# Performance work log

Hardware: AMD Instinct MI355X
Metric: run time of the kernel (lower is better)

Reference implementation:

```python
import jax, jax.numpy as jnp
import numpy as np

N_RBF = 20
CUTOFF = 5.0
LN_EPS = 1e-5


def setup_inputs() -> dict:
    key = jax.random.key(0)
    ks = jax.random.split(key, 16)
    N, E, F, H = 20000, 160000, 128, 4
    HF = H * F

    def lin_w(k, fin, fout):
        return (jax.random.normal(k, (fin, fout), jnp.float32) / np.sqrt(fin)).astype(jnp.float32)

    inp = {
        "s_j": jax.random.normal(ks[0], (N, F), jnp.float32),
        "dist": jax.random.uniform(ks[1], (E,), jnp.float32, 0.5, CUTOFF),
        "nbrs": jax.random.randint(ks[2], (E, 2), 0, N),
        # LayerNorm params
        "ln_g": jnp.ones((F,), jnp.float32),
        "ln_b": jnp.zeros((F,), jnp.float32),
        # q/k/v projections: feat_dim -> num_heads*feat_dim
        "Wq": lin_w(ks[3], F, HF), "bq": 0.01 * jax.random.normal(ks[4], (HF,), jnp.float32),
        "Wk": lin_w(ks[5], F, HF), "bk": 0.01 * jax.random.normal(ks[6], (HF,), jnp.float32),
        "Wv": lin_w(ks[7], F, HF), "bv": 0.01 * jax.random.normal(ks[8], (HF,), jnp.float32),
        # RBF -> distance filters dk/dv (Dense with swish activation)
        "dkW": lin_w(ks[9], N_RBF, HF), "dkb": 0.01 * jax.random.normal(ks[10], (HF,), jnp.float32),
        "dvW": lin_w(ks[11], N_RBF, HF), "dvb": 0.01 * jax.random.normal(ks[12], (HF,), jnp.float32),
        # final dense: num_heads*feat_dim -> 3*feat_dim
        "denseW": lin_w(ks[13], HF, 3 * F), "denseb": 0.01 * jax.random.normal(ks[14], (3 * F,), jnp.float32),
    }
    return inp


def reference(s_j, dist, nbrs, ln_g, ln_b, Wq, bq, Wk, bk, Wv, bv, dkW, dkb, dvW, dvb, denseW, denseb):
    F = s_j.shape[-1]
    HF = Wq.shape[-1]
    H = HF // F
    E = dist.shape[0]

    # LayerNorm over feature dim
    mu = s_j.mean(-1, keepdims=True)
    var = ((s_j - mu) ** 2).mean(-1, keepdims=True)
    inp = (s_j - mu) * jax.lax.rsqrt(var + LN_EPS) * ln_g + ln_b  # [N, F]

    # multi-head q/k/v: [N, H, F]
    q = (inp @ Wq + bq).reshape(-1, H, F)
    k = (inp @ Wk + bk).reshape(-1, H, F)
    v = (inp @ Wv + bv).reshape(-1, H, F)

    # Gaussian RBF expansion of distances: [E, n_rbf]
    centers = jnp.linspace(0.0, CUTOFF, N_RBF, dtype=jnp.float32)
    delta = CUTOFF / (N_RBF - 1)
    e_rbf = jnp.exp(-0.5 * ((dist[:, None] - centers) / delta) ** 2)

    # distance filters (Dense + swish): [E, H, F]
    dk = jax.nn.silu(e_rbf @ dkW + dkb).reshape(E, H, F)
    dv = jax.nn.silu(e_rbf @ dvW + dvb).reshape(E, H, F)

    i_idx, j_idx = nbrs[:, 0], nbrs[:, 1]

    # per-edge multi-head attention weight: silu(sum_f q_i * k_j * dk)
    attn = jax.nn.silu(jnp.einsum('ehf,ehf->eh', q[i_idx] * dk, k[j_idx]))  # [E, H]
    env = 0.5 * (jnp.cos(jnp.pi * dist / CUTOFF) + 1.0)  # cosine cutoff envelope [E]

    msg = (attn * env[:, None])[..., None] * v[j_idx] * dv  # [E, H, F]
    out = msg.reshape(E, HF) @ denseW + denseb  # [E, 3F]
    return out.reshape(E, 3, -1)
```

## Files before the change

### kernel.cpp

```cpp
#include <hip/hip_runtime.h>
#include <cstdint>
#include <cstddef>

typedef unsigned short u16;

#define F_DIM   128
#define HF_DIM  512
#define NRBF    20
#define NOUT    384

using bf16x8 = __attribute__((ext_vector_type(8))) __bf16;
using f32x4  = __attribute__((ext_vector_type(4))) float;

__device__ __forceinline__ float bf2f(u16 u){
    union { unsigned int i; float f; } v; v.i = ((unsigned int)u) << 16; return v.f;
}
__device__ __forceinline__ u16 f2bf(float f){
    union { float f; unsigned int i; } v; v.f = f;
    unsigned int x = v.i;
    unsigned int r = x + 0x7fffu + ((x >> 16) & 1u);
    return (u16)(r >> 16);
}
__device__ __forceinline__ float silu(float x){
    return x * __fdividef(1.0f, 1.0f + __expf(-x));
}

__global__ __launch_bounds__(256) void s0_packW(
    const float* __restrict__ dW, u16* __restrict__ Bp)
{
    const int t = blockIdx.x * 256 + threadIdx.x;
    if (t >= 24 * 16 * 64 * 8) return;
    const int j    = t & 7;
    const int lane = (t >> 3) & 63;
    const int ks   = (t >> 9) & 15;
    const int nt   = t >> 13;
    const int k = ks * 32 + ((lane >> 4) << 3) + j;
    const int n = nt * 16 + (lane & 15);
    Bp[t] = f2bf(dW[(size_t)k * NOUT + n]);
}

__global__ __launch_bounds__(128) void s1_ln(
    const float* __restrict__ s_j, const float* __restrict__ ln_g,
    const float* __restrict__ ln_b, float* __restrict__ inp, int N)
{
    __shared__ float ps[2], pss[2];
    const int n = blockIdx.x;
    const int f = threadIdx.x;
    float x = s_j[(size_t)n * F_DIM + f];
    float s = x, ss = x * x;
    #pragma unroll
    for (int o = 1; o < 64; o <<= 1){
        s  += __shfl_xor(s,  o);
        ss += __shfl_xor(ss, o);
    }
    const int wid = f >> 6;
    if ((f & 63) == 0){ ps[wid] = s; pss[wid] = ss; }
    __syncthreads();
    const float S  = ps[0] + ps[1];
    const float SS = pss[0] + pss[1];
    const float mu  = S * (1.f / 128.f);
    const float var = SS * (1.f / 128.f) - mu * mu;
    const float r   = rsqrtf(var + 1e-5f);
    inp[(size_t)n * F_DIM + f] = (x - mu) * r * ln_g[f] + ln_b[f];
}

__global__ __launch_bounds__(512) void s2_qkv(
    const float* __restrict__ inp,
    const float* __restrict__ Wq, const float* __restrict__ bq,
    const float* __restrict__ Wk, const float* __restrict__ bk,
    const float* __restrict__ Wv, const float* __restrict__ bv,
    u16* __restrict__ qo, u16* __restrict__ ko, u16* __restrict__ vo, int N)
{
    __shared__ float a[F_DIM];
    const int n = blockIdx.x;
    const int col = threadIdx.x;
    if (col < F_DIM) a[col] = inp[(size_t)n * F_DIM + col];
    __syncthreads();
    float aq = bq[col], ak = bk[col], av = bv[col];
    for (int k = 0; k < F_DIM; k++){
        const float x = a[k];
        aq += x * Wq[k * HF_DIM + col];
        ak += x * Wk[k * HF_DIM + col];
        av += x * Wv[k * HF_DIM + col];
    }
    qo[(size_t)n * HF_DIM + col] = f2bf(aq);
    ko[(size_t)n * HF_DIM + col] = f2bf(ak);
    vo[(size_t)n * HF_DIM + col] = f2bf(av);
}

__global__ __launch_bounds__(256) void s3_edge_dense(
    const float* __restrict__ dist, const int* __restrict__ nbrs,
    const u16* __restrict__ q_ws, const u16* __restrict__ k_ws, const u16* __restrict__ v_ws,
    const float* __restrict__ dkW, const float* __restrict__ dkb,
    const float* __restrict__ dvW, const float* __restrict__ dvb,
    const u16* __restrict__ Bp, const float* __restrict__ db,
    float* __restrict__ out, int E, int N)
{
    __shared__ __align__(16) u16 msg_s[32][520];
    __shared__ float rbf_sh[32][21];
    __shared__ float env_sh[32];
    const int tid = threadIdx.x;
    const int e0 = blockIdx.x * 32;

    if (tid < 32){
        int de = e0 + tid; if (de >= E) de = E - 1;
        float d = dist[de];
        env_sh[tid] = 0.5f * (__cosf(0.62831853071f * d) + 1.0f);
        const float delta = 5.0f / 19.0f;
        const float invd  = 19.0f / 5.0f;
        #pragma unroll
        for (int r = 0; r < NRBF; r++){
            float t = (d - delta * (float)r) * invd;
            rbf_sh[tid][r] = __expf(-0.5f * t * t);
        }
    }
    __syncthreads();

    {
        const int e_l = tid >> 3, sub = tid & 7;
        const int h = sub >> 1, half = sub & 1;
        const int fb = h * F_DIM + half * 64;
        int e = e0 + e_l; if (e >= E) e = E - 1;
        int i_idx = nbrs[2*e + 0];
        int j_idx = nbrs[2*e + 1];
        i_idx = (i_idx < 0) ? 0 : (i_idx >= N ? N-1 : i_idx);
        j_idx = (j_idx < 0) ? 0 : (j_idx >= N ? N-1 : j_idx);
        float rbf[NRBF];
        #pragma unroll
        for (int r = 0; r < NRBF; r++) rbf[r] = rbf_sh[e_l][r];
        const float env = env_sh[e_l];
        const u16* qrow = q_ws + (size_t)i_idx * HF_DIM + fb;
        const u16* krow = k_ws + (size_t)j_idx * HF_DIM + fb;
        const u16* vrow = v_ws + (size_t)j_idx * HF_DIM + fb;

        float attn = 0.f;
        for (int c = 0; c < 8; c++){
            const int f0 = c * 8;
            float a8[8];
            #pragma unroll
            for (int j = 0; j < 8; j++) a8[j] = dkb[fb + f0 + j];
            #pragma unroll
            for (int r = 0; r < NRBF; r++){
                const float rv = rbf[r];
                const float* wp = dkW + (size_t)r * HF_DIM + fb + f0;
                #pragma unroll
                for (int j = 0; j < 8; j++) a8[j] += rv * wp[j];
            }
            uint4 qu = *(const uint4*)(qrow + f0);
            uint4 ku = *(const uint4*)(krow + f0);
            const u16* qp = (const u16*)&qu;
            const u16* kp = (const u16*)&ku;
            #pragma unroll
            for (int j = 0; j < 8; j++)
                attn += bf2f(qp[j]) * silu(a8[j]) * bf2f(kp[j]);
        }
        attn += __shfl_xor(attn, 1);
        const float scale = silu(attn) * env;

        for (int c = 0; c < 8; c++){
            const int f0 = c * 8;
            float a8[8];
            #pragma unroll
            for (int j = 0; j < 8; j++) a8[j] = dvb[fb + f0 + j];
            #pragma unroll
            for (int r = 0; r < NRBF; r++){
                const float rv = rbf[r];
                const float* wp = dvW + (size_t)r * HF_DIM + fb + f0;
                #pragma unroll
                for (int j = 0; j < 8; j++) a8[j] += rv * wp[j];
            }
            uint4 vu = *(const uint4*)(vrow + f0);
            const u16* vp = (const u16*)&vu;
            u16 ov[8];
            #pragma unroll
            for (int j = 0; j < 8; j++)
                ov[j] = f2bf(scale * bf2f(vp[j]) * silu(a8[j]));
            *(uint4*)&msg_s[e_l][fb + f0] = *(const uint4*)ov;
        }
    }
    __syncthreads();

    {
        const int lane = tid & 63;
        const int wave = tid >> 6;
        const int am   = lane & 15;
        const int akb  = (lane >> 4) << 3;
        const int cn   = lane & 15;
        const int cr0  = (lane >> 4) << 2;

        f32x4 acc[2][6];
        #pragma unroll
        for (int nt = 0; nt < 6; nt++){
            const float bias = db[wave * 96 + nt * 16 + cn];
            acc[0][nt] = (f32x4){bias, bias, bias, bias};
            acc[1][nt] = acc[0][nt];
        }

        const u16* bbase = Bp + (size_t)(wave * 6) * (16 * 64 * 8);

        #pragma unroll 4
        for (int ks = 0; ks < 16; ks++){
            const bf16x8 a0 = *(const bf16x8*)&msg_s[am]     [(ks << 5) + akb];
            const bf16x8 a1 = *(const bf16x8*)&msg_s[16 + am][(ks << 5) + akb];
            #pragma unroll
            for (int nt = 0; nt < 6; nt++){
                const bf16x8 b = *(const bf16x8*)(bbase + (((nt * 16 + ks) * 64 + lane) << 3));
                acc[0][nt] = __builtin_amdgcn_mfma_f32_16x16x32_bf16(a0, b, acc[0][nt], 0, 0, 0);
                acc[1][nt] = __builtin_amdgcn_mfma_f32_16x16x32_bf16(a1, b, acc[1][nt], 0, 0, 0);
            }
        }

        #pragma unroll
        for (int mt = 0; mt < 2; mt++){
            #pragma unroll
            for (int r = 0; r < 4; r++){
                const int grow = e0 + mt * 16 + cr0 + r;
                if (grow < E){
                    float* op = out + (size_t)grow * NOUT + wave * 96 + cn;
                    #pragma unroll
                    for (int nt = 0; nt < 6; nt++)
                        op[nt * 16] = acc[mt][nt][r];
                }
            }
        }
    }
}

extern "C" void kernel_launch(void* const* d_in, const int* in_sizes, int n_in,
                              void* d_out, int out_size, void* d_ws, size_t ws_size,
                              hipStream_t stream)
{
    const float* s_j  = (const float*)d_in[0];
    const float* dist = (const float*)d_in[1];
    const int*   nbrs = (const int*)d_in[2];
    const float* ln_g = (const float*)d_in[3];
    const float* ln_b = (const float*)d_in[4];
    const float* Wq   = (const float*)d_in[5];
    const float* bq   = (const float*)d_in[6];
    const float* Wk   = (const float*)d_in[7];
    const float* bk   = (const float*)d_in[8];
    const float* Wv   = (const float*)d_in[9];
    const float* bv   = (const float*)d_in[10];
    const float* dkW  = (const float*)d_in[11];
    const float* dkb  = (const float*)d_in[12];
    const float* dvW  = (const float*)d_in[13];
    const float* dvb  = (const float*)d_in[14];
    const float* dW   = (const float*)d_in[15];
    const float* db   = (const float*)d_in[16];
    const int N = in_sizes[0] / F_DIM;
    const int E = in_sizes[1];
    (void)n_in; (void)out_size; (void)ws_size;

    char* ws = (char*)d_ws;
    size_t off = 0;
    auto walloc = [&](size_t bytes) -> void* {
        void* p = ws + off;
        off += (bytes + 255) & ~(size_t)255;
        return p;
    };
    float* inp_ws = (float*)walloc((size_t)N * F_DIM * 4);
    u16*   q_ws   = (u16*)walloc((size_t)N * HF_DIM * 2);
    u16*   k_ws   = (u16*)walloc((size_t)N * HF_DIM * 2);
    u16*   v_ws   = (u16*)walloc((size_t)N * HF_DIM * 2);
    u16*   Bp_ws  = (u16*)walloc((size_t)24 * 16 * 64 * 8 * 2);

    s0_packW<<<768, 256, 0, stream>>>(dW, Bp_ws);
    s1_ln<<<N, 128, 0, stream>>>(s_j, ln_g, ln_b, inp_ws, N);
    s2_qkv<<<N, 512, 0, stream>>>(inp_ws, Wq, bq, Wk, bk, Wv, bv,
                                  q_ws, k_ws, v_ws, N);
    s3_edge_dense<<<(E + 31)/32, 256, 0, stream>>>(
        dist, nbrs, q_ws, k_ws, v_ws,
        dkW, dkb, dvW, dvb, Bp_ws, db, (float*)d_out, E, N);
}
```

Measured before the change: 2.400 ms.

## Register-tile QKV projection and split edge kernel into message and dense passes

The QKV projection now processes 16 nodes per block with each thread computing two output columns, so each weight load is reused across many nodes instead of once per node. When workspace allows, the fused edge kernel is split into a message kernel that writes bf16 messages to global memory and a separate MFMA dense kernel with 512 threads. The q/k/v row loads are also hoisted ahead of the filter computation to overlap latency. The split adds a large intermediate global write and read in exchange for simpler, higher-occupancy kernels.

```diff
diff --git a/kernel.cpp b/kernel.cpp
--- a/kernel.cpp
+++ b/kernel.cpp
@@ -64,31 +64,204 @@
     inp[(size_t)n * F_DIM + f] = (x - mu) * r * ln_g[f] + ln_b[f];
 }
 
-__global__ __launch_bounds__(512) void s2_qkv(
+#define S2_NT 16
+__device__ __forceinline__ void s2_mat(
+    const float (*a_s)[F_DIM], const float* __restrict__ W,
+    const float* __restrict__ b, u16* __restrict__ o, int n0, int c0)
+{
+    float acc0[S2_NT], acc1[S2_NT];
+    const float b0 = b[c0], b1 = b[c0 + 1];
+    #pragma unroll
+    for (int n = 0; n < S2_NT; n++){ acc0[n] = b0; acc1[n] = b1; }
+    for (int k = 0; k < F_DIM; k += 4){
+        const float2 w0 = *(const float2*)(W + (size_t)(k+0) * HF_DIM + c0);
+        const float2 w1 = *(const float2*)(W + (size_t)(k+1) * HF_DIM + c0);
+        const float2 w2 = *(const float2*)(W + (size_t)(k+2) * HF_DIM + c0);
+        const float2 w3 = *(const float2*)(W + (size_t)(k+3) * HF_DIM + c0);
+        #pragma unroll
+        for (int n = 0; n < S2_NT; n++){
+            const float4 av = *(const float4*)&a_s[n][k];
+            acc0[n] += av.x*w0.x + av.y*w1.x + av.z*w2.x + av.w*w3.x;
+            acc1[n] += av.x*w0.y + av.y*w1.y + av.z*w2.y + av.w*w3.y;
+        }
+    }
+    #pragma unroll
+    for (int n = 0; n < S2_NT; n++){
+        const unsigned int pack =
+            (unsigned int)f2bf(acc0[n]) | ((unsigned int)f2bf(acc1[n]) << 16);
+        *(unsigned int*)(o + (size_t)(n0 + n) * HF_DIM + c0) = pack;
+    }
+}
+
+__global__ __launch_bounds__(256) void s2_qkv_t(
     const float* __restrict__ inp,
     const float* __restrict__ Wq, const float* __restrict__ bq,
     const float* __restrict__ Wk, const float* __restrict__ bk,
     const float* __restrict__ Wv, const float* __restrict__ bv,
     u16* __restrict__ qo, u16* __restrict__ ko, u16* __restrict__ vo, int N)
 {
-    __shared__ float a[F_DIM];
-    const int n = blockIdx.x;
-    const int col = threadIdx.x;
-    if (col < F_DIM) a[col] = inp[(size_t)n * F_DIM + col];
-    __syncthreads();
-    float aq = bq[col], ak = bk[col], av = bv[col];
-    for (int k = 0; k < F_DIM; k++){
-        const float x = a[k];
-        aq += x * Wq[k * HF_DIM + col];
-        ak += x * Wk[k * HF_DIM + col];
-        av += x * Wv[k * HF_DIM + col];
-    }
-    qo[(size_t)n * HF_DIM + col] = f2bf(aq);
-    ko[(size_t)n * HF_DIM + col] = f2bf(ak);
-    vo[(size_t)n * HF_DIM + col] = f2bf(av);
-}
-
-__global__ __launch_bounds__(256) void s3_edge_dense(
+    __shared__ float a_s[S2_NT][F_DIM];
+    const int tid = threadIdx.x;
+    const int n0 = blockIdx.x * S2_NT;
+    for (int i = tid; i < S2_NT * F_DIM / 4; i += 256)
+        ((float4*)a_s)[i] = ((const float4*)(inp + (size_t)n0 * F_DIM))[i];
+    __syncthreads();
+    const int c0 = tid * 2;
+    s2_mat(a_s, Wq, bq, qo, n0, c0);
+    s2_mat(a_s, Wk, bk, ko, n0, c0);
+    s2_mat(a_s, Wv, bv, vo, n0, c0);
+}
+
+__global__ __launch_bounds__(256) void s3a_edge_msg(
+    const float* __restrict__ dist, const int* __restrict__ nbrs,
+    const u16* __restrict__ q_ws, const u16* __restrict__ k_ws, const u16* __restrict__ v_ws,
+    const float* __restrict__ dkW, const float* __restrict__ dkb,
+    const float* __restrict__ dvW, const float* __restrict__ dvb,
+    u16* __restrict__ msg_g, int E, int N)
+{
+    __shared__ float rbf_sh[32][21];
+    __shared__ float env_sh[32];
+    const int tid = threadIdx.x;
+    const int e0 = blockIdx.x * 32;
+
+    if (tid < 32){
+        int de = e0 + tid; if (de >= E) de = E - 1;
+        float d = dist[de];
+        env_sh[tid] = 0.5f * (__cosf(0.62831853071f * d) + 1.0f);
+        const float delta = 5.0f / 19.0f;
+        const float invd  = 19.0f / 5.0f;
+        #pragma unroll
+        for (int r = 0; r < NRBF; r++){
+            float t = (d - delta * (float)r) * invd;
+            rbf_sh[tid][r] = __expf(-0.5f * t * t);
+        }
+    }
+    __syncthreads();
+
+    const int e_l = tid >> 3, sub = tid & 7;
+    const int h = sub >> 1, half = sub & 1;
+    const int fb = h * F_DIM + half * 64;
+    int e = e0 + e_l; if (e >= E) e = E - 1;
+    int i_idx = nbrs[2*e + 0];
+    int j_idx = nbrs[2*e + 1];
+    i_idx = (i_idx < 0) ? 0 : (i_idx >= N ? N-1 : i_idx);
+    j_idx = (j_idx < 0) ? 0 : (j_idx >= N ? N-1 : j_idx);
+    float rbf[NRBF];
+    #pragma unroll
+    for (int r = 0; r < NRBF; r++) rbf[r] = rbf_sh[e_l][r];
+    const float env = env_sh[e_l];
+    const u16* qrow = q_ws + (size_t)i_idx * HF_DIM + fb;
+    const u16* krow = k_ws + (size_t)j_idx * HF_DIM + fb;
+    const u16* vrow = v_ws + (size_t)j_idx * HF_DIM + fb;
+    u16* mrow = msg_g + (size_t)e * HF_DIM + fb;
+
+    float attn = 0.f;
+    for (int c = 0; c < 8; c++){
+        const int f0 = c * 8;
+        uint4 qu = *(const uint4*)(qrow + f0);
+        uint4 ku = *(const uint4*)(krow + f0);
+        float a8[8];
+        #pragma unroll
+        for (int j = 0; j < 8; j++) a8[j] = dkb[fb + f0 + j];
+        #pragma unroll
+        for (int r = 0; r < NRBF; r++){
+            const float rv = rbf[r];
+            const float* wp = dkW + (size_t)r * HF_DIM + fb + f0;
+            #pragma unroll
+            for (int j = 0; j < 8; j++) a8[j] += rv * wp[j];
+        }
+        const u16* qp = (const u16*)&qu;
+        const u16* kp = (const u16*)&ku;
+        #pragma unroll
+        for (int j = 0; j < 8; j++)
+            attn += bf2f(qp[j]) * silu(a8[j]) * bf2f(kp[j]);
+    }
+    attn += __shfl_xor(attn, 1);
+    const float scale = silu(attn) * env;
+
+    for (int c = 0; c < 8; c++){
+        const int f0 = c * 8;
+        uint4 vu = *(const uint4*)(vrow + f0);
+        float a8[8];
+        #pragma unroll
+        for (int j = 0; j < 8; j++) a8[j] = dvb[fb + f0 + j];
+        #pragma unroll
+        for (int r = 0; r < NRBF; r++){
+            const float rv = rbf[r];
+            const float* wp = dvW + (size_t)r * HF_DIM + fb + f0;
+            #pragma unroll
+            for (int j = 0; j < 8; j++) a8[j] += rv * wp[j];
+        }
+        const u16* vp = (const u16*)&vu;
+        u16 ov[8];
+        #pragma unroll
+        for (int j = 0; j < 8; j++)
+            ov[j] = f2bf(scale * bf2f(vp[j]) * silu(a8[j]));
+        *(uint4*)(mrow + f0) = *(const uint4*)ov;
+    }
+}
+
+__global__ __launch_bounds__(512) void s3b_dense(
+    const u16* __restrict__ msg_g, const u16* __restrict__ Bp,
+    const float* __restrict__ db, float* __restrict__ out, int E)
+{
+    __shared__ __align__(16) u16 msg_s[32][520];
+    const int tid = threadIdx.x;
+    const int e0 = blockIdx.x * 32;
+
+    for (int i = tid; i < 32 * 64; i += 512){
+        const int row = i >> 6, ch = i & 63;
+        int ge = e0 + row; if (ge >= E) ge = E - 1;
+        const uint4 d = *(const uint4*)(msg_g + (size_t)ge * HF_DIM + ch * 8);
+        *(uint4*)&msg_s[row][ch * 8] = d;
+    }
+    __syncthreads();
+
+    const int lane = tid & 63;
+    const int wave = tid >> 6;
+    const int am   = lane & 15;
+    const int akb  = (lane >> 4) << 3;
+    const int cn   = lane & 15;
+    const int cr0  = (lane >> 4) << 2;
+
+    f32x4 acc[2][3];
+    #pragma unroll
+    for (int nt = 0; nt < 3; nt++){
+        const float bias = db[wave * 48 + nt * 16 + cn];
+        acc[0][nt] = (f32x4){bias, bias, bias, bias};
+        acc[1][nt] = acc[0][nt];
+    }
+
+    const u16* bbase = Bp + (size_t)(wave * 3) * (16 * 64 * 8);
+
+    #pragma unroll 4
+    for (int ks = 0; ks < 16; ks++){
+        const bf16x8 a0 = *(const bf16x8*)&msg_s[am]     [(ks << 5) + akb];
+        const bf16x8 a1 = *(const bf16x8*)&msg_s[16 + am][(ks << 5) + akb];
+        #pragma unroll
+        for (int nt = 0; nt < 3; nt++){
+            const bf16x8 b = *(const bf16x8*)(bbase + (((nt * 16 + ks) * 64 + lane) << 3));
+            acc[0][nt] = __builtin_amdgcn_mfma_f32_16x16x32_bf16(a0, b, acc[0][nt], 0, 0, 0);
+            acc[1][nt] = __builtin_amdgcn_mfma_f32_16x16x32_bf16(a1, b, acc[1][nt], 0, 0, 0);
+        }
+    }
+
+    #pragma unroll
+    for (int mt = 0; mt < 2; mt++){
+        #pragma unroll
+        for (int r = 0; r < 4; r++){
+            const int grow = e0 + mt * 16 + cr0 + r;
+            if (grow < E){
+                float* op = out + (size_t)grow * NOUT + wave * 48 + cn;
+                #pragma unroll
+                for (int nt = 0; nt < 3; nt++)
+                    op[nt * 16] = acc[mt][nt][r];
+            }
+        }
+    }
+}
+
+__global__ __launch_bounds__(256) void s3_fused(
     const float* __restrict__ dist, const int* __restrict__ nbrs,
     const u16* __restrict__ q_ws, const u16* __restrict__ k_ws, const u16* __restrict__ v_ws,
     const float* __restrict__ dkW, const float* __restrict__ dkb,
@@ -115,7 +288,6 @@
         }
     }
     __syncthreads();
-
     {
         const int e_l = tid >> 3, sub = tid & 7;
         const int h = sub >> 1, half = sub & 1;
@@ -136,6 +308,8 @@
         float attn = 0.f;
         for (int c = 0; c < 8; c++){
             const int f0 = c * 8;
+            uint4 qu = *(const uint4*)(qrow + f0);
+            uint4 ku = *(const uint4*)(krow + f0);
             float a8[8];
             #pragma unroll
             for (int j = 0; j < 8; j++) a8[j] = dkb[fb + f0 + j];
@@ -146,8 +320,6 @@
                 #pragma unroll
                 for (int j = 0; j < 8; j++) a8[j] += rv * wp[j];
             }
-            uint4 qu = *(const uint4*)(qrow + f0);
-            uint4 ku = *(const uint4*)(krow + f0);
             const u16* qp = (const u16*)&qu;
             const u16* kp = (const u16*)&ku;
             #pragma unroll
@@ -159,6 +331,7 @@
 
         for (int c = 0; c < 8; c++){
             const int f0 = c * 8;
+            uint4 vu = *(const uint4*)(vrow + f0);
             float a8[8];
             #pragma unroll
             for (int j = 0; j < 8; j++) a8[j] = dvb[fb + f0 + j];
@@ -169,7 +342,6 @@
                 #pragma unroll
                 for (int j = 0; j < 8; j++) a8[j] += rv * wp[j];
             }
-            uint4 vu = *(const uint4*)(vrow + f0);
             const u16* vp = (const u16*)&vu;
             u16 ov[8];
             #pragma unroll
@@ -179,7 +351,6 @@
         }
     }
     __syncthreads();
-
     {
         const int lane = tid & 63;
         const int wave = tid >> 6;
@@ -195,9 +366,7 @@
             acc[0][nt] = (f32x4){bias, bias, bias, bias};
             acc[1][nt] = acc[0][nt];
         }
-
         const u16* bbase = Bp + (size_t)(wave * 6) * (16 * 64 * 8);
-
         #pragma unroll 4
         for (int ks = 0; ks < 16; ks++){
             const bf16x8 a0 = *(const bf16x8*)&msg_s[am]     [(ks << 5) + akb];
@@ -209,7 +378,6 @@
                 acc[1][nt] = __builtin_amdgcn_mfma_f32_16x16x32_bf16(a1, b, acc[1][nt], 0, 0, 0);
             }
         }
-
         #pragma unroll
         for (int mt = 0; mt < 2; mt++){
             #pragma unroll
@@ -249,7 +417,7 @@
     const float* db   = (const float*)d_in[16];
     const int N = in_sizes[0] / F_DIM;
     const int E = in_sizes[1];
-    (void)n_in; (void)out_size; (void)ws_size;
+    (void)n_in; (void)out_size;
 
     char* ws = (char*)d_ws;
     size_t off = 0;
@@ -263,12 +431,25 @@
     u16*   k_ws   = (u16*)walloc((size_t)N * HF_DIM * 2);
     u16*   v_ws   = (u16*)walloc((size_t)N * HF_DIM * 2);
     u16*   Bp_ws  = (u16*)walloc((size_t)24 * 16 * 64 * 8 * 2);
+    const size_t off_base = off;
+    u16*   msg_ws = (u16*)walloc((size_t)E * HF_DIM * 2);
+    const bool can_split = (ws_size >= off);
+    (void)off_base;
 
     s0_packW<<<768, 256, 0, stream>>>(dW, Bp_ws);
     s1_ln<<<N, 128, 0, stream>>>(s_j, ln_g, ln_b, inp_ws, N);
-    s2_qkv<<<N, 512, 0, stream>>>(inp_ws, Wq, bq, Wk, bk, Wv, bv,
-                                  q_ws, k_ws, v_ws, N);
-    s3_edge_dense<<<(E + 31)/32, 256, 0, stream>>>(
-        dist, nbrs, q_ws, k_ws, v_ws,
-        dkW, dkb, dvW, dvb, Bp_ws, db, (float*)d_out, E, N);
-}
+    s2_qkv_t<<<(N + S2_NT - 1)/S2_NT, 256, 0, stream>>>(
+        inp_ws, Wq, bq, Wk, bk, Wv, bv, q_ws, k_ws, v_ws, N);
+
+    if (can_split){
+        s3a_edge_msg<<<(E + 31)/32, 256, 0, stream>>>(
+            dist, nbrs, q_ws, k_ws, v_ws,
+            dkW, dkb, dvW, dvb, msg_ws, E, N);
+        s3b_dense<<<(E + 31)/32, 512, 0, stream>>>(
+            msg_ws, Bp_ws, db, (float*)d_out, E);
+    } else {
+        s3_fused<<<(E + 31)/32, 256, 0, stream>>>(
+            dist, nbrs, q_ws, k_ws, v_ws,
+            dkW, dkb, dvW, dvb, Bp_ws, db, (float*)d_out, E, N);
+    }
+}
```

Measured after the change: 2.093 ms. 1.15x faster.
